# Optimization experiments

Measured on AMD Instinct MI355X. Metric: run time of the kernel, lower is better.

The kernel has to match this reference:

```python
import jax, jax.numpy as jnp
import numpy as np

B, T, F_IN, H = 64, 256, 2048, 1024


def setup_inputs() -> dict:
    key = jax.random.key(0)
    ks = jax.random.split(key, 8)
    s = 1.0 / np.sqrt(H)
    return {
        "input_var": jax.random.normal(ks[0], (B, T, F_IN), dtype=jnp.float32),
        "input_lengths": jax.random.randint(ks[1], (B,), 1, T + 1, dtype=jnp.int32),
        "W_p": jax.random.uniform(ks[2], (H, F_IN), jnp.float32, -s, s),
        "b_p": jax.random.uniform(ks[3], (H,), jnp.float32, -s, s),
        "w_ih": jax.random.uniform(ks[4], (3 * H, H), jnp.float32, -s, s),
        "w_hh": jax.random.uniform(ks[5], (3 * H, H), jnp.float32, -s, s),
        "b_ih": jax.random.uniform(ks[6], (3 * H,), jnp.float32, -s, s),
        "b_hh": jax.random.uniform(ks[7], (3 * H,), jnp.float32, -s, s),
    }


def reference(input_var, input_lengths, W_p, b_p, w_ih, w_hh, b_ih, b_hh):
    # project video features: (B,T,F) -> (B,T,H)
    emb = jnp.einsum("btf,hf->bth", input_var, W_p) + b_p
    # precompute input-gate contributions for all timesteps: (B,T,3H)
    gx = jnp.einsum("bth,gh->btg", emb, w_ih) + b_ih
    gx_t = jnp.swapaxes(gx, 0, 1)  # time-major (T,B,3H)
    t_idx = jnp.arange(T)
    mask_t = (t_idx[:, None] < input_lengths[None, :])  # (T,B)

    def step(h, inp):
        gi, m = inp  # gi: (B,3H), m: (B,)
        gh = h @ w_hh.T + b_hh  # (B,3H)
        r = jax.nn.sigmoid(gi[:, :H] + gh[:, :H])
        z = jax.nn.sigmoid(gi[:, H:2 * H] + gh[:, H:2 * H])
        n = jnp.tanh(gi[:, 2 * H:] + r * gh[:, 2 * H:])
        h_new = (1.0 - z) * n + z * h
        m2 = m[:, None]
        h = jnp.where(m2, h_new, h)           # packed: hidden frozen past length
        y = jnp.where(m2, h_new, 0.0)         # pad_packed: zeros past length
        return h, y

    h0 = jnp.zeros((B, H), dtype=input_var.dtype)
    _, ys = jax.lax.scan(step, h0, (gx_t, mask_t))  # ys: (T,B,H)
    output = jnp.swapaxes(ys, 0, 1)  # (B,T,H)
    hidden = output[:, -1, :]
    return (output, hidden)
```

## Files before the change

### kernel.cpp

```cpp
#include <hip/hip_runtime.h>
#include <stdint.h>


typedef __bf16 bfx8 __attribute__((ext_vector_type(8)));
typedef float  f32x4 __attribute__((ext_vector_type(4)));
typedef unsigned u32x4 __attribute__((ext_vector_type(4)));
typedef unsigned long long ull;

__global__ void cvt_bf16(const float* __restrict__ in, __bf16* __restrict__ out, int n8) {
    for (int i = blockIdx.x * blockDim.x + threadIdx.x; i < n8; i += gridDim.x * blockDim.x) {
        float4 a = ((const float4*)in)[2 * i];
        float4 b = ((const float4*)in)[2 * i + 1];
        union { __bf16 h[8]; uint4 v; } u;
        u.h[0] = (__bf16)a.x; u.h[1] = (__bf16)a.y; u.h[2] = (__bf16)a.z; u.h[3] = (__bf16)a.w;
        u.h[4] = (__bf16)b.x; u.h[5] = (__bf16)b.y; u.h[6] = (__bf16)b.z; u.h[7] = (__bf16)b.w;
        ((uint4*)out)[i] = u.v;
    }
}

__device__ __forceinline__ void g2l16(const void* g, void* l) {
    __builtin_amdgcn_global_load_lds(
        (__attribute__((address_space(1))) void*)g,
        (__attribute__((address_space(3))) void*)l,
        16, 0, 0);
}

template <bool OUTBF16>
__global__ __launch_bounds__(256)
void gemm_bt(const __bf16* __restrict__ A, const __bf16* __restrict__ W,
             const float* __restrict__ bias, void* __restrict__ C,
             int M, int N, int K)
{
    __shared__ __bf16 As[128 * 32];
    __shared__ __bf16 Ws[128 * 32];
    const int tid  = threadIdx.x;
    const int wave = tid >> 6, lane = tid & 63;
    const int q = lane >> 4, r15 = lane & 15;
    const int n0 = blockIdx.x << 7, m0 = blockIdx.y << 7;
    const int wm = (wave >> 1) << 6, wn = (wave & 1) << 6;
    const size_t Ks = (size_t)K;
    f32x4 acc[4][4] = {};

    for (int k0 = 0; k0 < K; k0 += 32) {
        __syncthreads();
#pragma unroll
        for (int i = 0; i < 2; ++i) {
            int o  = (((i << 2) + wave) << 10);
            int ob = o + (lane << 4);
            int row = ob >> 6, colb = ob & 63;
            g2l16((const char*)A + ((size_t)(m0 + row) * Ks + k0) * 2 + colb, (char*)As + o);
            g2l16((const char*)W + ((size_t)(n0 + row) * Ks + k0) * 2 + colb, (char*)Ws + o);
        }
        __syncthreads();

        bfx8 af[4], wf[4];
#pragma unroll
        for (int mt = 0; mt < 4; ++mt)
            af[mt] = *(const bfx8*)&As[((wm + (mt << 4) + r15) << 5) + (q << 3)];
#pragma unroll
        for (int nt = 0; nt < 4; ++nt)
            wf[nt] = *(const bfx8*)&Ws[((wn + (nt << 4) + r15) << 5) + (q << 3)];
#pragma unroll
        for (int mt = 0; mt < 4; ++mt)
#pragma unroll
            for (int nt = 0; nt < 4; ++nt)
                acc[mt][nt] = __builtin_amdgcn_mfma_f32_16x16x32_bf16(af[mt], wf[nt], acc[mt][nt], 0, 0, 0);
    }

#pragma unroll
    for (int nt = 0; nt < 4; ++nt) {
        int col = n0 + wn + (nt << 4) + r15;
        float bv = bias[col];
#pragma unroll
        for (int mt = 0; mt < 4; ++mt) {
#pragma unroll
            for (int i = 0; i < 4; ++i) {
                int rrow = m0 + wm + (mt << 4) + (q << 2) + i;
                float v = acc[mt][nt][i] + bv;
                if (OUTBF16) ((__bf16*)C)[(size_t)rrow * N + col] = (__bf16)v;
                else         ((float*)C)[(size_t)rrow * N + col]  = v;
            }
        }
    }
}

__device__ __forceinline__ float sigm(float x) { return 1.f / (1.f + __expf(-x)); }
__device__ __forceinline__ float tanh_f(float x) { float e = __expf(2.f * x); return 1.f - 2.f / (e + 1.f); }

#define RP 1032

__global__ __launch_bounds__(256, 1)
void rnn_kernel(const float* __restrict__ gx, const int* __restrict__ lens,
                const __bf16* __restrict__ whhb, const float* __restrict__ b_hh,
                char* __restrict__ hbuf,
                float* __restrict__ out,
                unsigned* __restrict__ flags)
{
    __shared__ __bf16 hs[16 * RP];
    __shared__ float  ghs2[3 * 4 * 256];

    const int tid  = threadIdx.x;
    const int wave = tid >> 6, lane = tid & 63;
    const int q = lane >> 4, r15 = lane & 15;
    const int bb = (blockIdx.x & 7) >> 1;
    const int bj = ((blockIdx.x >> 3) << 1) | (blockIdx.x & 1);

    bfx8 Bf[3][8];
#pragma unroll
    for (int g = 0; g < 3; ++g)
#pragma unroll
        for (int kk = 0; kk < 8; ++kk)
            Bf[g][kk] = *(const bfx8*)(whhb
                + ((size_t)((g << 10) + (bj << 4) + r15) << 10)
                + (wave << 8) + (kk << 5) + (q << 3));

    const int m_ = tid >> 4, jj_ = tid & 15;
    const int bglob = (bb << 4) + m_;
    const int jglob = (bj << 4) + jj_;
    const float bhr = b_hh[jglob], bhz = b_hh[1024 + jglob], bhn = b_hh[2048 + jglob];
    const int mylen = lens[bglob];
    const int pd   = (tid & 127) >> 1;
    const int pblk = ((pd >> 1) << 3) | (bb << 1) | (pd & 1);
    const unsigned* fpoll = &flags[pblk << 4];

    const float* gp = gx + (size_t)bglob * 256 * 3072 + jglob;
    float gir = gp[0], giz = gp[1024], gin = gp[2048];
    float hstate = 0.f;

    for (int t = 0; t < 256; ++t) {
        if (t > 0) {
            unsigned tgt = (unsigned)t;
            while (__hip_atomic_load(fpoll, __ATOMIC_RELAXED, __HIP_MEMORY_SCOPE_AGENT) < tgt)
                __builtin_amdgcn_s_sleep(1);
            asm volatile("" ::: "memory");
        }
        {
            const char* sb = hbuf + ((t & 1) << 17) + (bb << 15) + (tid << 4);
            u32x4 r0, r1, r2, r3, r4, r5, r6, r7;
            asm volatile(
                "global_load_dwordx4 %0, %8, off sc1\n\t"
                "global_load_dwordx4 %1, %9, off sc1\n\t"
                "global_load_dwordx4 %2, %10, off sc1\n\t"
                "global_load_dwordx4 %3, %11, off sc1\n\t"
                "global_load_dwordx4 %4, %12, off sc1\n\t"
                "global_load_dwordx4 %5, %13, off sc1\n\t"
                "global_load_dwordx4 %6, %14, off sc1\n\t"
                "global_load_dwordx4 %7, %15, off sc1\n\t"
                "s_waitcnt vmcnt(0)"
                : "=&v"(r0), "=&v"(r1), "=&v"(r2), "=&v"(r3),
                  "=&v"(r4), "=&v"(r5), "=&v"(r6), "=&v"(r7)
                : "v"(sb),          "v"(sb + 4096),  "v"(sb + 8192),  "v"(sb + 12288),
                  "v"(sb + 16384),  "v"(sb + 20480), "v"(sb + 24576), "v"(sb + 28672)
                : "memory");
            const int colb = (tid & 127) << 4;
            const int mh = tid >> 7;
            char* hsb = (char*)hs;
            *(u32x4*)(hsb + (2 * 0 + mh) * 2064 + colb) = r0;
            *(u32x4*)(hsb + (2 * 1 + mh) * 2064 + colb) = r1;
            *(u32x4*)(hsb + (2 * 2 + mh) * 2064 + colb) = r2;
            *(u32x4*)(hsb + (2 * 3 + mh) * 2064 + colb) = r3;
            *(u32x4*)(hsb + (2 * 4 + mh) * 2064 + colb) = r4;
            *(u32x4*)(hsb + (2 * 5 + mh) * 2064 + colb) = r5;
            *(u32x4*)(hsb + (2 * 6 + mh) * 2064 + colb) = r6;
            *(u32x4*)(hsb + (2 * 7 + mh) * 2064 + colb) = r7;
        }
        __syncthreads();

        {
            f32x4 a0 = {0.f, 0.f, 0.f, 0.f}, a1 = a0, a2 = a0;
            const __bf16* hrow = &hs[r15 * RP + (wave << 8)];
#pragma unroll
            for (int kk = 0; kk < 8; ++kk) {
                bfx8 a = *(const bfx8*)(hrow + (kk << 5) + (q << 3));
                a0 = __builtin_amdgcn_mfma_f32_16x16x32_bf16(a, Bf[0][kk], a0, 0, 0, 0);
                a1 = __builtin_amdgcn_mfma_f32_16x16x32_bf16(a, Bf[1][kk], a1, 0, 0, 0);
                a2 = __builtin_amdgcn_mfma_f32_16x16x32_bf16(a, Bf[2][kk], a2, 0, 0, 0);
            }
#pragma unroll
            for (int i2 = 0; i2 < 4; ++i2) {
                int di = (((q << 2) + i2) << 4) + r15;
                ghs2[(wave << 8) + di]        = a0[i2];
                ghs2[1024 + (wave << 8) + di] = a1[i2];
                ghs2[2048 + (wave << 8) + di] = a2[i2];
            }
        }
        __syncthreads();

        float ghr = ghs2[tid] + ghs2[256 + tid] + ghs2[512 + tid] + ghs2[768 + tid] + bhr;
        float ghz = ghs2[1024 + tid] + ghs2[1280 + tid] + ghs2[1536 + tid] + ghs2[1792 + tid] + bhz;
        float ghn = ghs2[2048 + tid] + ghs2[2304 + tid] + ghs2[2560 + tid] + ghs2[2816 + tid] + bhn;
        float rg = sigm(gir + ghr);
        float zg = sigm(giz + ghz);
        float ng = tanh_f(gin + rg * ghn);
        float hnew = (1.f - zg) * ng + zg * hstate;
        bool mk = t < mylen;
        hstate = mk ? hnew : hstate;
        float y = mk ? hnew : 0.f;

        if (t < 255) {
            union { unsigned short us; __bf16 h; } cv; cv.h = (__bf16)hstate;
            unsigned hb = cv.us;
            unsigned nb = (unsigned)__shfl_xor((int)hb, 1);
            if (!(tid & 1)) {
                unsigned dv = hb | (nb << 16);
                unsigned* hw = (unsigned*)(hbuf + (((t + 1) & 1) << 17)
                             + (bglob << 11) + ((bj << 4) + jj_) * 2);
                __hip_atomic_store(hw, dv, __ATOMIC_RELAXED, __HIP_MEMORY_SCOPE_AGENT);
            }
            __syncthreads();
            if (tid == 0)
                __hip_atomic_store(&flags[blockIdx.x << 4], (unsigned)(t + 1),
                                   __ATOMIC_RELAXED, __HIP_MEMORY_SCOPE_AGENT);
            out[(size_t)(bglob * 256 + t) * 1024 + jglob] = y;
            gp += 3072;
            gir = gp[0]; giz = gp[1024]; gin = gp[2048];
        } else {
            out[(size_t)(bglob * 256 + t) * 1024 + jglob] = y;
            out[(size_t)(64 * 256) * 1024 + ((size_t)bglob << 10) + jglob] = y;
        }
    }
}

extern "C" void kernel_launch(void* const* d_in, const int* in_sizes, int n_in,
                              void* d_out, int out_size, void* d_ws, size_t ws_size,
                              hipStream_t stream) {
    const float* input = (const float*)d_in[0];
    const int*   lens  = (const int*)d_in[1];
    const float* W_p   = (const float*)d_in[2];
    const float* b_p   = (const float*)d_in[3];
    const float* w_ih  = (const float*)d_in[4];
    const float* w_hh  = (const float*)d_in[5];
    const float* b_ih  = (const float*)d_in[6];
    const float* b_hh  = (const float*)d_in[7];
    float* out = (float*)d_out;
    char* ws = (char*)d_ws;

    __bf16* Xb   = (__bf16*)(ws + 0);
    __bf16* Wpb  = (__bf16*)(ws + 67108864);
    __bf16* wihb = (__bf16*)(ws + 71303168);
    __bf16* whhb = (__bf16*)(ws + 77594624);
    __bf16* embb = (__bf16*)(ws + 83886080);
    float*  gx   = (float*) (ws + 117440512);
    char* hbuf   = ws + 318767104;
    unsigned* flags = (unsigned*)(ws + 319029248);

    hipMemsetAsync(ws + 318767104, 0, 262144 + 16384, stream);

    cvt_bf16<<<4096, 256, 0, stream>>>(input, Xb, 33554432 / 8);
    cvt_bf16<<<1024, 256, 0, stream>>>(W_p,  Wpb, 2097152 / 8);
    cvt_bf16<<<1536, 256, 0, stream>>>(w_ih, wihb, 3145728 / 8);
    cvt_bf16<<<1536, 256, 0, stream>>>(w_hh, whhb, 3145728 / 8);

    gemm_bt<true><<<dim3(8, 128), 256, 0, stream>>>(Xb, Wpb, b_p, embb, 16384, 1024, 2048);
    gemm_bt<false><<<dim3(24, 128), 256, 0, stream>>>(embb, wihb, b_ih, gx, 16384, 3072, 1024);

    rnn_kernel<<<256, 256, 0, stream>>>(gx, lens, whhb, b_hh, hbuf, out, flags);
}
```

Measured before the change: 1.041 ms.

## Replace 128x128 GEMM with 256x256 double-buffered pipelined MFMA kernel

Swaps the simple 128x128-tile, 256-thread GEMM for a 256x256-tile, 512-thread kernel. It uses 128KB of LDS as a double buffer over 64-wide K tiles, with XOR-swizzled LDS layout, interleaved prefetch of the next tiles between MFMA phases, s_setprio, and an XCD-aware block remap. The aim is more data reuse per tile, hiding global-load latency and avoiding LDS bank conflicts in the two projection GEMMs. In exchange it raises register and LDS pressure to one block per CU and adds manual waitcnt/barrier choreography that must stay correct.

Result: faster. 978.4 us (-6.1%).

```diff
diff --git a/kernel.cpp b/kernel.cpp
--- a/kernel.cpp
+++ b/kernel.cpp
@@ -25,60 +25,164 @@
         16, 0, 0);
 }
 
+
+__device__ __forceinline__ void stage_half16(const char* mat, int row0, size_t Kb, int tk,
+                                             char* ldsHalf, int sr, int scb, int wave) {
+    const char* s0 = mat + (size_t)(row0 + sr) * Kb + ((size_t)tk << 7) + scb;
+    g2l16(s0, ldsHalf + (wave << 10));
+    g2l16(s0 + (Kb << 6), ldsHalf + 8192 + (wave << 10));
+}
+
+#define MFMA16 __builtin_amdgcn_mfma_f32_16x16x32_bf16
+
 template <bool OUTBF16>
-__global__ __launch_bounds__(256)
-void gemm_bt(const __bf16* __restrict__ A, const __bf16* __restrict__ W,
+__global__ __launch_bounds__(512)
+void gemm256(const __bf16* __restrict__ A, const __bf16* __restrict__ W,
              const float* __restrict__ bias, void* __restrict__ C,
              int M, int N, int K)
 {
-    __shared__ __bf16 As[128 * 32];
-    __shared__ __bf16 Ws[128 * 32];
+    __shared__ char smem[131072];
     const int tid  = threadIdx.x;
     const int wave = tid >> 6, lane = tid & 63;
     const int q = lane >> 4, r15 = lane & 15;
-    const int n0 = blockIdx.x << 7, m0 = blockIdx.y << 7;
-    const int wm = (wave >> 1) << 6, wn = (wave & 1) << 6;
-    const size_t Ks = (size_t)K;
-    f32x4 acc[4][4] = {};
-
-    for (int k0 = 0; k0 < K; k0 += 32) {
-        __syncthreads();
-#pragma unroll
-        for (int i = 0; i < 2; ++i) {
-            int o  = (((i << 2) + wave) << 10);
-            int ob = o + (lane << 4);
-            int row = ob >> 6, colb = ob & 63;
-            g2l16((const char*)A + ((size_t)(m0 + row) * Ks + k0) * 2 + colb, (char*)As + o);
-            g2l16((const char*)W + ((size_t)(n0 + row) * Ks + k0) * 2 + colb, (char*)Ws + o);
-        }
-        __syncthreads();
-
-        bfx8 af[4], wf[4];
-#pragma unroll
-        for (int mt = 0; mt < 4; ++mt)
-            af[mt] = *(const bfx8*)&As[((wm + (mt << 4) + r15) << 5) + (q << 3)];
-#pragma unroll
-        for (int nt = 0; nt < 4; ++nt)
-            wf[nt] = *(const bfx8*)&Ws[((wn + (nt << 4) + r15) << 5) + (q << 3)];
-#pragma unroll
-        for (int mt = 0; mt < 4; ++mt)
-#pragma unroll
-            for (int nt = 0; nt < 4; ++nt)
-                acc[mt][nt] = __builtin_amdgcn_mfma_f32_16x16x32_bf16(af[mt], wf[nt], acc[mt][nt], 0, 0, 0);
-    }
-
-#pragma unroll
-    for (int nt = 0; nt < 4; ++nt) {
-        int col = n0 + wn + (nt << 4) + r15;
-        float bv = bias[col];
-#pragma unroll
-        for (int mt = 0; mt < 4; ++mt) {
+    const int wm = wave >> 2, wn = wave & 3;
+
+    const int nbx = N >> 8;
+    const int nwg = (M >> 8) * nbx;
+    const int cpx = nwg >> 3;
+    const int wg  = (blockIdx.x & 7) * cpx + (blockIdx.x >> 3);
+    const int m0  = (wg / nbx) << 8, n0 = (wg % nbx) << 8;
+    const size_t Kb = (size_t)K << 1;
+    const int NT = K >> 6;
+
+    const int sr  = tid >> 3;
+    const int scb = ((tid ^ (tid >> 3)) & 7) << 4;
+    const int sx  = r15 & 7;
+    const int la0 = r15 * 128 + ((q ^ sx) << 4);
+    const int la1 = r15 * 128 + (((q | 4) ^ sx) << 4);
+
+    const char* Ac = (const char*)A;
+    const char* Wc = (const char*)W;
+
+#pragma unroll
+    for (int t = 0; t < 2; ++t) {
+        char* ab = smem + (t << 15);
+        char* bb = smem + 65536 + (t << 15);
+        stage_half16(Ac, m0,       Kb, t, ab,         sr, scb, wave);
+        stage_half16(Ac, m0 + 128, Kb, t, ab + 16384, sr, scb, wave);
+        stage_half16(Wc, n0,       Kb, t, bb,         sr, scb, wave);
+        stage_half16(Wc, n0 + 128, Kb, t, bb + 16384, sr, scb, wave);
+    }
+    asm volatile("s_waitcnt vmcnt(8)" ::: "memory");
+    __builtin_amdgcn_s_barrier();
+
+    f32x4 acc[8][4] = {};
+
+    for (int t = 0; t < NT; ++t) {
+        const int bsel = t & 1;
+        const char* Ab = smem + (bsel << 15) + (wm << 14);
+        const char* Bb = smem + 65536 + (bsel << 15) + ((wn >> 1) << 14) + ((wn & 1) << 13);
+        const int t2 = t + 2;
+        const bool st = t2 < NT;
+
+        bfx8 aw[4][2], b01[2][2], b23[2][2];
+
+#pragma unroll
+        for (int m = 0; m < 4; ++m) {
+            aw[m][0] = *(const bfx8*)(Ab + (m << 11) + la0);
+            aw[m][1] = *(const bfx8*)(Ab + (m << 11) + la1);
+        }
+#pragma unroll
+        for (int n = 0; n < 2; ++n) {
+            b01[n][0] = *(const bfx8*)(Bb + (n << 11) + la0);
+            b01[n][1] = *(const bfx8*)(Bb + (n << 11) + la1);
+        }
+        __builtin_amdgcn_s_barrier();
+        asm volatile("s_waitcnt lgkmcnt(0)" ::: "memory");
+        __builtin_amdgcn_s_setprio(1);
+#pragma unroll
+        for (int m = 0; m < 4; ++m)
+#pragma unroll
+            for (int n = 0; n < 2; ++n) {
+                acc[m][n] = MFMA16(aw[m][0], b01[n][0], acc[m][n], 0, 0, 0);
+                acc[m][n] = MFMA16(aw[m][1], b01[n][1], acc[m][n], 0, 0, 0);
+            }
+        __builtin_amdgcn_s_setprio(0);
+        __builtin_amdgcn_s_barrier();
+
+#pragma unroll
+        for (int n = 0; n < 2; ++n) {
+            b23[n][0] = *(const bfx8*)(Bb + ((n + 2) << 11) + la0);
+            b23[n][1] = *(const bfx8*)(Bb + ((n + 2) << 11) + la1);
+        }
+        if (st) {
+            char* bb = smem + 65536 + (bsel << 15);
+            stage_half16(Wc, n0,       Kb, t2, bb,         sr, scb, wave);
+            stage_half16(Wc, n0 + 128, Kb, t2, bb + 16384, sr, scb, wave);
+        }
+        __builtin_amdgcn_s_barrier();
+        asm volatile("s_waitcnt lgkmcnt(0)" ::: "memory");
+        __builtin_amdgcn_s_setprio(1);
+#pragma unroll
+        for (int m = 0; m < 4; ++m)
+#pragma unroll
+            for (int n = 0; n < 2; ++n) {
+                acc[m][n + 2] = MFMA16(aw[m][0], b23[n][0], acc[m][n + 2], 0, 0, 0);
+                acc[m][n + 2] = MFMA16(aw[m][1], b23[n][1], acc[m][n + 2], 0, 0, 0);
+            }
+        __builtin_amdgcn_s_setprio(0);
+        __builtin_amdgcn_s_barrier();
+
+#pragma unroll
+        for (int m = 0; m < 4; ++m) {
+            aw[m][0] = *(const bfx8*)(Ab + 8192 + (m << 11) + la0);
+            aw[m][1] = *(const bfx8*)(Ab + 8192 + (m << 11) + la1);
+        }
+        if (st) {
+            char* ab = smem + (bsel << 15);
+            stage_half16(Ac, m0,       Kb, t2, ab,         sr, scb, wave);
+            stage_half16(Ac, m0 + 128, Kb, t2, ab + 16384, sr, scb, wave);
+        }
+        __builtin_amdgcn_s_barrier();
+        asm volatile("s_waitcnt lgkmcnt(0)" ::: "memory");
+        __builtin_amdgcn_s_setprio(1);
+#pragma unroll
+        for (int m = 0; m < 4; ++m)
+#pragma unroll
+            for (int n = 0; n < 2; ++n) {
+                acc[m + 4][n + 2] = MFMA16(aw[m][0], b23[n][0], acc[m + 4][n + 2], 0, 0, 0);
+                acc[m + 4][n + 2] = MFMA16(aw[m][1], b23[n][1], acc[m + 4][n + 2], 0, 0, 0);
+            }
+        __builtin_amdgcn_s_setprio(0);
+        __builtin_amdgcn_s_barrier();
+
+        if (t < NT - 2) asm volatile("s_waitcnt vmcnt(8)" ::: "memory");
+        else            asm volatile("s_waitcnt vmcnt(0)" ::: "memory");
+        __builtin_amdgcn_s_barrier();
+        __builtin_amdgcn_s_setprio(1);
+#pragma unroll
+        for (int m = 0; m < 4; ++m)
+#pragma unroll
+            for (int n = 0; n < 2; ++n) {
+                acc[m + 4][n] = MFMA16(aw[m][0], b01[n][0], acc[m + 4][n], 0, 0, 0);
+                acc[m + 4][n] = MFMA16(aw[m][1], b01[n][1], acc[m + 4][n], 0, 0, 0);
+            }
+        __builtin_amdgcn_s_setprio(0);
+        __builtin_amdgcn_s_barrier();
+    }
+
+#pragma unroll
+    for (int nf = 0; nf < 4; ++nf) {
+        const int col = n0 + (wn << 6) + (nf << 4) + r15;
+        const float bv = bias[col];
+#pragma unroll
+        for (int mf = 0; mf < 8; ++mf) {
 #pragma unroll
             for (int i = 0; i < 4; ++i) {
-                int rrow = m0 + wm + (mt << 4) + (q << 2) + i;
-                float v = acc[mt][nt][i] + bv;
-                if (OUTBF16) ((__bf16*)C)[(size_t)rrow * N + col] = (__bf16)v;
-                else         ((float*)C)[(size_t)rrow * N + col]  = v;
+                const int row = m0 + (wm << 7) + (mf << 4) + (q << 2) + i;
+                const float v = acc[mf][nf][i] + bv;
+                if (OUTBF16) ((__bf16*)C)[(size_t)row * N + col] = (__bf16)v;
+                else         ((float*)C)[(size_t)row * N + col]  = v;
             }
         }
     }
@@ -251,8 +355,8 @@
     cvt_bf16<<<1536, 256, 0, stream>>>(w_ih, wihb, 3145728 / 8);
     cvt_bf16<<<1536, 256, 0, stream>>>(w_hh, whhb, 3145728 / 8);
 
-    gemm_bt<true><<<dim3(8, 128), 256, 0, stream>>>(Xb, Wpb, b_p, embb, 16384, 1024, 2048);
-    gemm_bt<false><<<dim3(24, 128), 256, 0, stream>>>(embb, wihb, b_ih, gx, 16384, 3072, 1024);
+    gemm256<true><<<dim3(256), 512, 0, stream>>>(Xb, Wpb, b_p, embb, 16384, 1024, 2048);
+    gemm256<false><<<dim3(768), 512, 0, stream>>>(embb, wihb, b_ih, gx, 16384, 3072, 1024);
 
     rnn_kernel<<<256, 256, 0, stream>>>(gx, lens, whhb, b_hh, hbuf, out, flags);
 }
```
